# Kernel tuning notes

Hardware: AMD Instinct MI355X
Metric: run time of the kernel (lower is better)

## Reference

```python
import jax, jax.numpy as jnp
import numpy as np

T_BINS = 1000  # max_time_bins
N_HEADS = 8
BIN = 64


def _ln(x, g, b):
    m = x.mean(-1, keepdims=True)
    v = ((x - m) ** 2).mean(-1, keepdims=True)
    return (x - m) / jnp.sqrt(v + 1e-5) * g + b


def _time_attn(h, td, mask, wq, bq, wk, bk, wv, bv, wo, bo, temb):
    # h: [B,S,D], td: [B,S] float, mask: [B,S] bool
    B, S, D = h.shape
    dk = D // N_HEADS
    q = (h @ wq + bq).reshape(B, S, N_HEADS, dk)
    k = (h @ wk + bk).reshape(B, S, N_HEADS, dk)
    v = (h @ wv + bv).reshape(B, S, N_HEADS, dk)
    scores = jnp.einsum('bqhd,bkhd->bhqk', q, k) / jnp.sqrt(jnp.float32(dk))
    tb = jnp.clip(td.astype(jnp.int32), 0, T_BINS - 1)
    bias = temb[tb].transpose(0, 2, 1)[:, :, None, :]  # [B,H,1,S], key-position bias
    scores = jnp.where(mask[:, None, None, :], scores + bias, -1e9)
    attn = jax.nn.softmax(scores, axis=-1)
    ctx = jnp.einsum('bhqk,bkhd->bqhd', attn, v).reshape(B, S, D)
    return ctx @ wo + bo


def _forward(x, time_deltas,
             emb_event, emb_rel, emb_abs,
             iq_w, iq_b, ik_w, ik_b, iv_w, iv_b, io_w, io_b, i_temb, i_g, i_bt,
             eq_w, eq_b, ek_w, ek_b, ev_w, ev_b, eo_w, eo_b, e_temb, e_g, e_bt,
             w1, b1, w2, b2):
    B, S = x.shape
    NB = S // BIN  # S chosen as a multiple of bin_size -> no padding
    mask = x != 0  # padding_idx = 0
    ee = emb_event.at[0].set(0.0)  # padding_idx row is zero
    rel_bins = jnp.clip(time_deltas.astype(jnp.int32), 0, T_BINS - 1)
    abs_t = jnp.cumsum(jnp.clip(time_deltas, 0.0, None), axis=1)
    abs_bins = jnp.clip(abs_t.astype(jnp.int32), 0, T_BINS - 1)
    h = ee[x] + emb_rel[rel_bins] + emb_abs[abs_bins]  # [B,S,D]
    D = h.shape[-1]
    # intra-bin attention over [B*NB, BIN]
    hi = h.reshape(B * NB, BIN, D)
    ti = time_deltas.reshape(B * NB, BIN)
    mi = mask.reshape(B * NB, BIN)
    hi = _ln(_time_attn(hi, ti, mi, iq_w, iq_b, ik_w, ik_b, iv_w, iv_b, io_w, io_b, i_temb), i_g, i_bt)
    hi = hi.reshape(B, NB, BIN, D)
    # mean pool per bin over valid tokens
    mb = mask.reshape(B, NB, BIN)
    w = mb[..., None].astype(h.dtype)
    denom = jnp.maximum(w.sum(2), 1.0)
    bin_repr = (hi * w).sum(2) / denom  # [B,NB,D]
    bin_mask = mb.any(2)
    abs_masked = jnp.where(mb, abs_t.reshape(B, NB, BIN), 0.0)
    bin_abs = abs_masked.max(2)
    bin_rel = jnp.concatenate(
        [jnp.zeros((B, 1), h.dtype), jnp.maximum(bin_abs[:, 1:] - bin_abs[:, :-1], 0.0)], axis=1)
    h_inter = _ln(_time_attn(bin_repr, bin_rel, bin_mask,
                             eq_w, eq_b, ek_w, ek_b, ev_w, ev_b, eo_w, eo_b, e_temb), e_g, e_bt)
    last_idx = jnp.clip(bin_mask.sum(1) - 1, 0, None)
    last = h_inter[jnp.arange(B), last_idx]  # [B,D]
    return jax.nn.sigmoid(jax.nn.relu(last @ w1 + b1) @ w2 + b2)  # [B,1]


def setup_inputs() -> dict:
    key = jax.random.key(0)
    ks = jax.random.split(key, 24)
    B, S, D, V = 8, 4096, 512, 20000
    sc = 1.0 / np.sqrt(D)
    f32 = jnp.float32
    inp = {
        'x': jax.random.randint(ks[0], (B, S), 0, V),
        'time_deltas': jax.random.uniform(ks[1], (B, S), f32) * 10.0,
        'emb_event': jax.random.normal(ks[2], (V, D), f32) * 0.02,
        'emb_rel': jax.random.normal(ks[3], (T_BINS, D), f32) * 0.02,
        'emb_abs': jax.random.normal(ks[4], (T_BINS, D), f32) * 0.02,
    }
    names = ['iq', 'ik', 'iv', 'io', 'eq', 'ek', 'ev', 'eo']
    for i, n in enumerate(names):
        inp[n + '_w'] = jax.random.normal(ks[5 + i], (D, D), f32) * sc
        inp[n + '_b'] = jnp.zeros((D,), f32)
    inp['i_temb'] = jax.random.normal(ks[13], (T_BINS, N_HEADS), f32) * 0.02
    inp['e_temb'] = jax.random.normal(ks[14], (T_BINS, N_HEADS), f32) * 0.02
    inp['i_g'] = jnp.ones((D,), f32); inp['i_bt'] = jnp.zeros((D,), f32)
    inp['e_g'] = jnp.ones((D,), f32); inp['e_bt'] = jnp.zeros((D,), f32)
    inp['w1'] = jax.random.normal(ks[15], (D, D // 2), f32) * sc
    inp['b1'] = jnp.zeros((D // 2,), f32)
    inp['w2'] = jax.random.normal(ks[16], (D // 2, 1), f32) * np.sqrt(2.0 / D)
    inp['b2'] = jnp.zeros((1,), f32)
    return inp


def reference(x, time_deltas, emb_event, emb_rel, emb_abs,
              iq_w, iq_b, ik_w, ik_b, iv_w, iv_b, io_w, io_b, i_temb, i_g, i_bt,
              eq_w, eq_b, ek_w, ek_b, ev_w, ev_b, eo_w, eo_b, e_temb, e_g, e_bt,
              w1, b1, w2, b2):
    return _forward(x, time_deltas, emb_event, emb_rel, emb_abs,
                    iq_w, iq_b, ik_w, ik_b, iv_w, iv_b, io_w, io_b, i_temb, i_g, i_bt,
                    eq_w, eq_b, ek_w, ek_b, ev_w, ev_b, eo_w, eo_b, e_temb, e_g, e_bt,
                    w1, b1, w2, b2)
```

## Files before the change

### kernel.cpp

```cpp
#include <hip/hip_runtime.h>


typedef __attribute__((ext_vector_type(8))) short bf16x8;
typedef __attribute__((ext_vector_type(4))) float f32x4;
typedef __attribute__((ext_vector_type(4))) int i32x4;

#define DEVI __device__ __forceinline__

DEVI unsigned short f2bf(float f) {
  union { float f; unsigned u; } v; v.f = f;
  unsigned r = v.u + 0x7FFFu + ((v.u >> 16) & 1u);
  return (unsigned short)(r >> 16);
}
DEVI float bf2f(unsigned short u) {
  union { unsigned u; float f; } v; v.u = ((unsigned)u) << 16; return v.f;
}

#define GLOAD_LDS16(gp, lp) \
  __builtin_amdgcn_global_load_lds((const __attribute__((address_space(1))) void*)(gp), \
                                   (__attribute__((address_space(3))) void*)(lp), 16, 0, 0)

struct TPackArgs { const float* s[8]; unsigned short* d[8];
                   const float* bs[6]; float* bd[2]; };

__global__ __launch_bounds__(256) void k_tpack8(TPackArgs args) {
  __shared__ float tile[64][65];
  if (blockIdx.x == 512) {
    int t = threadIdx.x;
    for (int i = t; i < 1536; i += 256) {
      int sel = i >> 9, r = i & 511;
      args.bd[0][i] = args.bs[sel][r];
      args.bd[1][i] = args.bs[3 + sel][r];
    }
    return;
  }
  int mat = blockIdx.x >> 6;
  int tl = blockIdx.x & 63;
  const float* W = args.s[mat];
  unsigned short* Wt = args.d[mat];
  int n0 = (tl & 7) << 6, k0 = (tl >> 3) << 6;
  int t = threadIdx.x, j = t & 63, i0 = t >> 6;
#pragma unroll
  for (int rr = 0; rr < 16; ++rr) {
    int i = rr * 4 + i0;
    tile[i][j] = W[(size_t)(k0 + i) * 512 + n0 + j];
  }
  __syncthreads();
#pragma unroll
  for (int rr = 0; rr < 16; ++rr) {
    int i = rr * 4 + i0;
    Wt[(size_t)(n0 + i) * 512 + k0 + j] = f2bf(tile[j][i]);
  }
}

__global__ __launch_bounds__(64) void k_time(const float* __restrict__ td, const int* __restrict__ x,
    float* __restrict__ abs_t, float* __restrict__ bin_rel, int* __restrict__ bin_mask,
    int* __restrict__ last_idx) {
  __shared__ float tds[4096];
  __shared__ int xs[4096];
  int b = blockIdx.x, lane = threadIdx.x;
  const f32x4* tp = (const f32x4*)(td + (size_t)b * 4096);
  const i32x4* xp = (const i32x4*)(x + (size_t)b * 4096);
  for (int j = lane; j < 1024; j += 64) {
    f32x4 v = tp[j];
#pragma unroll
    for (int c = 0; c < 4; ++c) v[c] = fmaxf(v[c], 0.f);
    *(f32x4*)&tds[j * 4] = v;
    *(i32x4*)&xs[j * 4] = xp[j];
  }
  __syncthreads();
  float s = 0.f;
  for (int i = 0; i < 64; ++i) s += tds[lane * 64 + i];
  float pre = s;
#pragma unroll
  for (int off = 1; off < 64; off <<= 1) {
    float n = __shfl_up(pre, off, 64);
    if (lane >= off) pre += n;
  }
  float a = pre - s;
  float am = 0.f; int anyv = 0;
  for (int i = 0; i < 64; ++i) {
    a += tds[lane * 64 + i];
    tds[lane * 64 + i] = a;
    if (xs[lane * 64 + i] != 0) { am = fmaxf(am, a); anyv = 1; }
  }
  __syncthreads();
  float* out = abs_t + (size_t)b * 4096;
  for (int j = lane; j < 1024; j += 64)
    *(f32x4*)&out[j * 4] = *(const f32x4*)&tds[j * 4];
  float prev = __shfl_up(am, 1, 64);
  bin_rel[b * 64 + lane] = (lane == 0) ? 0.f : fmaxf(am - prev, 0.f);
  bin_mask[b * 64 + lane] = anyv;
  unsigned long long bal = __ballot(anyv != 0);
  if (lane == 0) last_idx[b] = max(__popcll(bal) - 1, 0);
}

__global__ __launch_bounds__(256) void k_embed(const int* __restrict__ x, const float* __restrict__ td,
    const float* __restrict__ abs_t, const float* __restrict__ ee, const float* __restrict__ er,
    const float* __restrict__ ea, unsigned short* __restrict__ h) {
  int t = threadIdx.x;
  int lane = t & 63;
  int c0 = lane * 8;
#pragma unroll
  for (int it = 0; it < 4; ++it) {
    int tok = blockIdx.x * 16 + it * 4 + (t >> 6);
    int xi = x[tok];
    int rb = (int)td[tok]; rb = min(max(rb, 0), 999);
    int ab = (int)abs_t[tok]; ab = min(max(ab, 0), 999);
    const f32x4* pr = (const f32x4*)(er + (size_t)rb * 512 + c0);
    const f32x4* pa = (const f32x4*)(ea + (size_t)ab * 512 + c0);
    f32x4 s0 = pr[0] + pa[0];
    f32x4 s1 = pr[1] + pa[1];
    if (xi != 0) {
      const f32x4* pe = (const f32x4*)(ee + (size_t)xi * 512 + c0);
      s0 += pe[0]; s1 += pe[1];
    }
    bf16x8 o;
#pragma unroll
    for (int i = 0; i < 4; ++i) { o[i] = (short)f2bf(s0[i]); o[4 + i] = (short)f2bf(s1[i]); }
    *(bf16x8*)(h + (size_t)tok * 512 + c0) = o;
  }
}

DEVI bf16x8 lds_frag64(const unsigned short* buf, int row, int c) {
  return *(const bf16x8*)&buf[row * 64 + ((c ^ (row & 7)) << 3)];
}

__global__ __launch_bounds__(256) void k_g128(const unsigned short* __restrict__ A,
    const unsigned short* __restrict__ Wt, const float* __restrict__ bias,
    unsigned short* __restrict__ Cout, int N, int tiles_n) {
  __shared__ unsigned short As[128 * 64];
  __shared__ unsigned short Bs[128 * 64];
  int bid = blockIdx.x;
  { int q = (int)gridDim.x >> 3; bid = (bid & 7) * q + (bid >> 3); }
  int by = bid / tiles_n, bx = bid % tiles_n;
  int m0 = by << 7, n0 = bx << 7;
  int t = threadIdx.x;
  int lane = t & 63, w = t >> 6;
  int wm = w >> 1, wn = w & 1;
  int l15 = lane & 15, l4 = lane >> 4;
  f32x4 acc[4][4] = {};
  for (int k0 = 0; k0 < 512; k0 += 64) {
    __syncthreads();
#pragma unroll
    for (int l = 0; l < 4; ++l) {
      int pos = l * 256 + t;
      int row = pos >> 3, g = (pos & 7) ^ (row & 7);
      GLOAD_LDS16(&A[(size_t)(m0 + row) * 512 + k0 + g * 8], &As[pos * 8]);
    }
#pragma unroll
    for (int l = 0; l < 4; ++l) {
      int pos = l * 256 + t;
      int row = pos >> 3, g = (pos & 7) ^ (row & 7);
      GLOAD_LDS16(&Wt[(size_t)(n0 + row) * 512 + k0 + g * 8], &Bs[pos * 8]);
    }
    __syncthreads();
#pragma unroll
    for (int ks = 0; ks < 2; ++ks) {
      bf16x8 af[4], bb[4];
#pragma unroll
      for (int i = 0; i < 4; ++i) {
        af[i] = lds_frag64(As, wm * 64 + i * 16 + l15, ks * 4 + l4);
        bb[i] = lds_frag64(Bs, wn * 64 + i * 16 + l15, ks * 4 + l4);
      }
#pragma unroll
      for (int i = 0; i < 4; ++i)
#pragma unroll
        for (int j = 0; j < 4; ++j)
          acc[i][j] = __builtin_amdgcn_mfma_f32_16x16x32_bf16(af[i], bb[j], acc[i][j], 0, 0, 0);
    }
  }
#pragma unroll
  for (int i = 0; i < 4; ++i) {
    int rowb = m0 + wm * 64 + i * 16 + ((lane >> 4) << 2);
#pragma unroll
    for (int j = 0; j < 4; ++j) {
      int col = n0 + wn * 64 + j * 16 + (lane & 15);
      float bv = bias[col];
#pragma unroll
      for (int r = 0; r < 4; ++r)
        Cout[(size_t)(rowb + r) * N + col] = f2bf(acc[i][j][r] + bv);
    }
  }
}

__global__ __launch_bounds__(512, 2) void k_oproj(const unsigned short* __restrict__ ctx,
    const unsigned short* __restrict__ WoT, const float* __restrict__ bo,
    const int* __restrict__ x, const float* __restrict__ g, const float* __restrict__ bt,
    unsigned short* __restrict__ bin_repr) {
  __shared__ unsigned short As[128 * 64];
  __shared__ unsigned short Bs[512 * 64];
  int bid = blockIdx.x;
  { int q = (int)gridDim.x >> 3; bid = (bid & 7) * q + (bid >> 3); }
  int m0 = bid << 7;
  int t = threadIdx.x;
  int lane = t & 63, w = t >> 6;
  int l15 = lane & 15, l4 = lane >> 4;

  f32x4 acc[8][4] = {};
  for (int k0 = 0; k0 < 512; k0 += 64) {
    __syncthreads();
#pragma unroll
    for (int l = 0; l < 2; ++l) {
      int pos = l * 512 + t;
      int row = pos >> 3, gg = (pos & 7) ^ (row & 7);
      GLOAD_LDS16(&ctx[(size_t)(m0 + row) * 512 + k0 + gg * 8], &As[pos * 8]);
    }
#pragma unroll
    for (int l = 0; l < 8; ++l) {
      int pos = l * 512 + t;
      int row = pos >> 3, gg = (pos & 7) ^ (row & 7);
      GLOAD_LDS16(&WoT[(size_t)row * 512 + k0 + gg * 8], &Bs[pos * 8]);
    }
    __syncthreads();
#pragma unroll
    for (int ks = 0; ks < 2; ++ks) {
      bf16x8 af[8], bb[4];
#pragma unroll
      for (int i = 0; i < 8; ++i) af[i] = lds_frag64(As, i * 16 + l15, ks * 4 + l4);
#pragma unroll
      for (int j = 0; j < 4; ++j) bb[j] = lds_frag64(Bs, w * 64 + j * 16 + l15, ks * 4 + l4);
#pragma unroll
      for (int i = 0; i < 8; ++i)
#pragma unroll
        for (int j = 0; j < 4; ++j)
          acc[i][j] = __builtin_amdgcn_mfma_f32_16x16x32_bf16(af[i], bb[j], acc[i][j], 0, 0, 0);
    }
  }

  __syncthreads();
  float* red   = (float*)&As[0];
  float* meanL = red + 128 * 9;
  float* rstdL = meanL + 128;
  int*   valL  = (int*)(rstdL + 128);
  int*   cntL  = valL + 128;

  int cols[4]; float bov[4], gv[4], bv[4];
#pragma unroll
  for (int j = 0; j < 4; ++j) {
    cols[j] = w * 64 + j * 16 + l15;
    bov[j] = bo[cols[j]]; gv[j] = g[cols[j]]; bv[j] = bt[cols[j]];
  }
  if (t < 128) {
    int v = (x[m0 + t] != 0) ? 1 : 0;
    valL[t] = v;
    unsigned long long bal = __ballot(v != 0);
    if ((t & 63) == 0) cntL[t >> 6] = __popcll(bal);
  }
#pragma unroll
  for (int i = 0; i < 8; ++i)
#pragma unroll
    for (int r = 0; r < 4; ++r) {
      float s = (acc[i][0][r] + bov[0]) + (acc[i][1][r] + bov[1]) +
                (acc[i][2][r] + bov[2]) + (acc[i][3][r] + bov[3]);
#pragma unroll
      for (int off = 1; off < 16; off <<= 1) s += __shfl_xor(s, off, 64);
      if (l15 == 0) red[(i * 16 + l4 * 4 + r) * 9 + w] = s;
    }
  __syncthreads();
  if (t < 128) {
    float m = 0.f;
#pragma unroll
    for (int ww = 0; ww < 8; ++ww) m += red[t * 9 + ww];
    meanL[t] = m * (1.f / 512.f);
  }
  __syncthreads();
#pragma unroll
  for (int i = 0; i < 8; ++i)
#pragma unroll
    for (int r = 0; r < 4; ++r) {
      float m = meanL[i * 16 + l4 * 4 + r];
      float s = 0.f;
#pragma unroll
      for (int j = 0; j < 4; ++j) { float d = acc[i][j][r] + bov[j] - m; s += d * d; }
#pragma unroll
      for (int off = 1; off < 16; off <<= 1) s += __shfl_xor(s, off, 64);
      if (l15 == 0) red[(i * 16 + l4 * 4 + r) * 9 + w] = s;
    }
  __syncthreads();
  if (t < 128) {
    float vsum = 0.f;
#pragma unroll
    for (int ww = 0; ww < 8; ++ww) vsum += red[t * 9 + ww];
    rstdL[t] = rsqrtf(vsum * (1.f / 512.f) + 1e-5f);
  }
  __syncthreads();
  float p0[4] = {0.f, 0.f, 0.f, 0.f}, p1[4] = {0.f, 0.f, 0.f, 0.f};
#pragma unroll
  for (int i = 0; i < 8; ++i)
#pragma unroll
    for (int r = 0; r < 4; ++r) {
      int row = i * 16 + l4 * 4 + r;
      if (valL[row]) {
        float m = meanL[row], rs = rstdL[row];
#pragma unroll
        for (int j = 0; j < 4; ++j) {
          float y = (acc[i][j][r] + bov[j] - m) * rs * gv[j] + bv[j];
          if (i < 4) p0[j] += y; else p1[j] += y;
        }
      }
    }
#pragma unroll
  for (int j = 0; j < 4; ++j) {
    p0[j] += __shfl_xor(p0[j], 16, 64); p0[j] += __shfl_xor(p0[j], 32, 64);
    p1[j] += __shfl_xor(p1[j], 16, 64); p1[j] += __shfl_xor(p1[j], 32, 64);
  }
  float d0 = 1.f / fmaxf((float)cntL[0], 1.f);
  float d1 = 1.f / fmaxf((float)cntL[1], 1.f);
  if (l4 == 0) {
    int binr = (m0 >> 6);
#pragma unroll
    for (int j = 0; j < 4; ++j) {
      bin_repr[(size_t)binr * 512 + cols[j]]       = f2bf(p0[j] * d0);
      bin_repr[(size_t)(binr + 1) * 512 + cols[j]] = f2bf(p1[j] * d1);
    }
  }
}

__global__ __launch_bounds__(256) void k_gemm(const unsigned short* __restrict__ A,
    const unsigned short* __restrict__ Wt, const float* __restrict__ bias,
    unsigned short* __restrict__ Cout, int N, int tiles_n) {
  __shared__ unsigned short As[128 * 72];
  __shared__ unsigned short Bs[128 * 72];
  int bx = blockIdx.x % tiles_n;
  int by = blockIdx.x / tiles_n;
  int m0 = by << 7, n0 = bx << 7;
  int t = threadIdx.x;
  int lane = t & 63, w = t >> 6;
  int wm = w >> 1, wn = w & 1;
  f32x4 acc[4][4] = {};
  for (int k0 = 0; k0 < 512; k0 += 64) {
    __syncthreads();
#pragma unroll
    for (int i = 0; i < 4; ++i) {
      int idx = t + i * 256;
      int row = idx >> 3, seg = idx & 7;
      *(bf16x8*)&As[row * 72 + seg * 8] = *(const bf16x8*)&A[(size_t)(m0 + row) * 512 + k0 + seg * 8];
      *(bf16x8*)&Bs[row * 72 + seg * 8] = *(const bf16x8*)&Wt[(size_t)(n0 + row) * 512 + k0 + seg * 8];
    }
    __syncthreads();
#pragma unroll
    for (int ks = 0; ks < 2; ++ks) {
      bf16x8 af[4], bb[4];
#pragma unroll
      for (int i = 0; i < 4; ++i) {
        af[i] = *(const bf16x8*)&As[(wm * 64 + i * 16 + (lane & 15)) * 72 + ks * 32 + (lane >> 4) * 8];
        bb[i] = *(const bf16x8*)&Bs[(wn * 64 + i * 16 + (lane & 15)) * 72 + ks * 32 + (lane >> 4) * 8];
      }
#pragma unroll
      for (int i = 0; i < 4; ++i)
#pragma unroll
        for (int j = 0; j < 4; ++j)
          acc[i][j] = __builtin_amdgcn_mfma_f32_16x16x32_bf16(af[i], bb[j], acc[i][j], 0, 0, 0);
    }
  }
#pragma unroll
  for (int i = 0; i < 4; ++i) {
    int rowb = m0 + wm * 64 + i * 16 + ((lane >> 4) << 2);
#pragma unroll
    for (int j = 0; j < 4; ++j) {
      int col = n0 + wn * 64 + j * 16 + (lane & 15);
      float bv = bias[col];
#pragma unroll
      for (int r = 0; r < 4; ++r)
        Cout[(size_t)(rowb + r) * N + col] = f2bf(acc[i][j][r] + bv);
    }
  }
}

__global__ __launch_bounds__(256) void k_attn(const unsigned short* __restrict__ qkv,
    const float* __restrict__ td, const int* __restrict__ validv,
    const float* __restrict__ temb, unsigned short* __restrict__ ctx) {
  __shared__ float bias_s[4][64];
  __shared__ int valid_s[64];
  __shared__ unsigned short P_s[4][64][72];
  __shared__ unsigned short Vt_s[4][64][72];
  int blk = blockIdx.x >> 1, hg = blockIdx.x & 1;
  int t = threadIdx.x, hl = t >> 6, lane = t & 63;
  int h = hg * 4 + hl;
  size_t base = (size_t)blk * 64;
  if (t < 64) {
    valid_s[t] = (validv[base + t] != 0) ? 1 : 0;
    int tb = (int)td[base + t];
    tb = min(max(tb, 0), 999);
#pragma unroll
    for (int hh = 0; hh < 4; ++hh) bias_s[hh][t] = temb[tb * 8 + hg * 4 + hh];
  }
  {
    const unsigned short* vp = qkv + (base + lane) * 1536 + 1024 + h * 64;
#pragma unroll
    for (int f8 = 0; f8 < 8; ++f8) {
      bf16x8 v8 = *(const bf16x8*)(vp + f8 * 8);
#pragma unroll
      for (int j = 0; j < 8; ++j) Vt_s[hl][f8 * 8 + j][lane] = (unsigned short)v8[j];
    }
  }
  __syncthreads();
  bf16x8 qa[2][4], kb[2][4];
#pragma unroll
  for (int ks = 0; ks < 2; ++ks)
#pragma unroll
    for (int i = 0; i < 4; ++i) {
      int row = i * 16 + (lane & 15);
      int kk = ks * 32 + (lane >> 4) * 8;
      qa[ks][i] = *(const bf16x8*)&qkv[(base + row) * 1536 + h * 64 + kk];
      kb[ks][i] = *(const bf16x8*)&qkv[(base + row) * 1536 + 512 + h * 64 + kk];
    }
  f32x4 acc[4][4] = {};
#pragma unroll
  for (int ks = 0; ks < 2; ++ks)
#pragma unroll
    for (int i = 0; i < 4; ++i)
#pragma unroll
      for (int j = 0; j < 4; ++j)
        acc[i][j] = __builtin_amdgcn_mfma_f32_16x16x32_bf16(qa[ks][i], kb[ks][j], acc[i][j], 0, 0, 0);
  float invs[4][4];
#pragma unroll
  for (int i = 0; i < 4; ++i) {
#pragma unroll
    for (int r = 0; r < 4; ++r) {
      float sv[4];
#pragma unroll
      for (int j = 0; j < 4; ++j) {
        int key = j * 16 + (lane & 15);
        float s = acc[i][j][r] * 0.125f;
        sv[j] = valid_s[key] ? (s + bias_s[hl][key]) : -1e9f;
      }
      float m = fmaxf(fmaxf(sv[0], sv[1]), fmaxf(sv[2], sv[3]));
#pragma unroll
      for (int off = 1; off < 16; off <<= 1) m = fmaxf(m, __shfl_xor(m, off, 64));
      float p[4], sum = 0.f;
#pragma unroll
      for (int j = 0; j < 4; ++j) { p[j] = __expf(sv[j] - m); sum += p[j]; }
#pragma unroll
      for (int off = 1; off < 16; off <<= 1) sum += __shfl_xor(sum, off, 64);
      invs[i][r] = 1.f / sum;
      int row = i * 16 + ((lane >> 4) << 2) + r;
#pragma unroll
      for (int j = 0; j < 4; ++j) P_s[hl][row][j * 16 + (lane & 15)] = f2bf(p[j]);
    }
  }
  __syncthreads();
  f32x4 acc2[4][4] = {};
#pragma unroll
  for (int ks = 0; ks < 2; ++ks) {
    bf16x8 pa[4], vb[4];
    int kk = ks * 32 + (lane >> 4) * 8;
#pragma unroll
    for (int i = 0; i < 4; ++i) {
      pa[i] = *(const bf16x8*)&P_s[hl][i * 16 + (lane & 15)][kk];
      vb[i] = *(const bf16x8*)&Vt_s[hl][i * 16 + (lane & 15)][kk];
    }
#pragma unroll
    for (int i = 0; i < 4; ++i)
#pragma unroll
      for (int j = 0; j < 4; ++j)
        acc2[i][j] = __builtin_amdgcn_mfma_f32_16x16x32_bf16(pa[i], vb[j], acc2[i][j], 0, 0, 0);
  }
#pragma unroll
  for (int i = 0; i < 4; ++i) {
    int rowb = i * 16 + ((lane >> 4) << 2);
#pragma unroll
    for (int j = 0; j < 4; ++j) {
      int col = h * 64 + j * 16 + (lane & 15);
#pragma unroll
      for (int r = 0; r < 4; ++r)
        ctx[(base + rowb + r) * 512 + col] = f2bf(acc2[i][j][r] * invs[i][r]);
    }
  }
}

__global__ __launch_bounds__(256) void k_final(const unsigned short* __restrict__ proj2,
    const int* __restrict__ last_idx, const float* __restrict__ g, const float* __restrict__ bt,
    const float* __restrict__ w1, const float* __restrict__ b1,
    const float* __restrict__ w2, const float* __restrict__ b2, float* __restrict__ outp) {
  __shared__ float row_s[512];
  __shared__ float red_s[4];
  __shared__ float red2_s[4];
  int b = blockIdx.x, t = threadIdx.x;
  const unsigned short* rp = proj2 + (size_t)(b * 64 + last_idx[b]) * 512;
  float v0 = bf2f(rp[t]), v1 = bf2f(rp[t + 256]);
  float s = v0 + v1;
#pragma unroll
  for (int off = 1; off < 64; off <<= 1) s += __shfl_xor(s, off, 64);
  if ((t & 63) == 0) red_s[t >> 6] = s;
  __syncthreads();
  float mean = (red_s[0] + red_s[1] + red_s[2] + red_s[3]) * (1.f / 512.f);
  float d0 = v0 - mean, d1 = v1 - mean;
  float vs = d0 * d0 + d1 * d1;
#pragma unroll
  for (int off = 1; off < 64; off <<= 1) vs += __shfl_xor(vs, off, 64);
  if ((t & 63) == 0) red2_s[t >> 6] = vs;
  __syncthreads();
  float rstd = rsqrtf((red2_s[0] + red2_s[1] + red2_s[2] + red2_s[3]) * (1.f / 512.f) + 1e-5f);
  row_s[t]       = d0 * rstd * g[t]       + bt[t];
  row_s[t + 256] = d1 * rstd * g[t + 256] + bt[t + 256];
  __syncthreads();
  float acc = b1[t];
  for (int k = 0; k < 512; ++k) acc += row_s[k] * w1[(size_t)k * 256 + t];
  float hv = fmaxf(acc, 0.f) * w2[t];
#pragma unroll
  for (int off = 1; off < 64; off <<= 1) hv += __shfl_xor(hv, off, 64);
  if ((t & 63) == 0) red_s[t >> 6] = hv;
  __syncthreads();
  if (t == 0) {
    float o = red_s[0] + red_s[1] + red_s[2] + red_s[3] + b2[0];
    outp[b] = 1.f / (1.f + __expf(-o));
  }
}

extern "C" void kernel_launch(void* const* d_in, const int* in_sizes, int n_in,
                              void* d_out, int out_size, void* d_ws, size_t ws_size,
                              hipStream_t stream) {
  const int*   x    = (const int*)d_in[0];
  const float* td   = (const float*)d_in[1];
  const float* ee   = (const float*)d_in[2];
  const float* er   = (const float*)d_in[3];
  const float* ea   = (const float*)d_in[4];
  const float* iq_w = (const float*)d_in[5];  const float* iq_b = (const float*)d_in[6];
  const float* ik_w = (const float*)d_in[7];  const float* ik_b = (const float*)d_in[8];
  const float* iv_w = (const float*)d_in[9];  const float* iv_b = (const float*)d_in[10];
  const float* io_w = (const float*)d_in[11]; const float* io_b = (const float*)d_in[12];
  const float* eq_w = (const float*)d_in[13]; const float* eq_b = (const float*)d_in[14];
  const float* ek_w = (const float*)d_in[15]; const float* ek_b = (const float*)d_in[16];
  const float* ev_w = (const float*)d_in[17]; const float* ev_b = (const float*)d_in[18];
  const float* eo_w = (const float*)d_in[19]; const float* eo_b = (const float*)d_in[20];
  const float* i_temb = (const float*)d_in[21];
  const float* e_temb = (const float*)d_in[22];
  const float* i_g  = (const float*)d_in[23]; const float* i_bt = (const float*)d_in[24];
  const float* e_g  = (const float*)d_in[25]; const float* e_bt = (const float*)d_in[26];
  const float* w1   = (const float*)d_in[27]; const float* b1   = (const float*)d_in[28];
  const float* w2   = (const float*)d_in[29]; const float* b2   = (const float*)d_in[30];

  char* ws = (char*)d_ws;
  size_t off = 0;
  auto alloc = [&](size_t nb) { size_t r = off; off += (nb + 255) & ~(size_t)255; return r; };
  float* abs_t    = (float*)(ws + alloc((size_t)32768 * 4));
  float* bin_rel  = (float*)(ws + alloc(512 * 4));
  int*   bin_mask = (int*)(ws + alloc(512 * 4));
  int*   last_idx = (int*)(ws + alloc(64));
  unsigned short* wqkv_i = (unsigned short*)(ws + alloc((size_t)1536 * 512 * 2));
  unsigned short* wo_i   = (unsigned short*)(ws + alloc((size_t)512 * 512 * 2));
  unsigned short* wqkv_e = (unsigned short*)(ws + alloc((size_t)1536 * 512 * 2));
  unsigned short* wo_e   = (unsigned short*)(ws + alloc((size_t)512 * 512 * 2));
  float* bqkv_i = (float*)(ws + alloc(1536 * 4));
  float* bqkv_e = (float*)(ws + alloc(1536 * 4));
  unsigned short* hbuf = (unsigned short*)(ws + alloc((size_t)32768 * 512 * 2));
  unsigned short* qkvbuf = (unsigned short*)(ws + alloc((size_t)32768 * 1536 * 2));
  unsigned short* bin_repr = (unsigned short*)(ws + alloc((size_t)512 * 512 * 2));
  char* small = ws + alloc((size_t)512 * 1536 * 2);
  unsigned short* qkv2 = (unsigned short*)small;
  unsigned short* proj2 = (unsigned short*)small;
  unsigned short* ctx2 = (unsigned short*)(ws + alloc((size_t)512 * 512 * 2));

  TPackArgs tp;
  tp.s[0] = iq_w; tp.d[0] = wqkv_i;
  tp.s[1] = ik_w; tp.d[1] = wqkv_i + (size_t)512 * 512;
  tp.s[2] = iv_w; tp.d[2] = wqkv_i + (size_t)1024 * 512;
  tp.s[3] = io_w; tp.d[3] = wo_i;
  tp.s[4] = eq_w; tp.d[4] = wqkv_e;
  tp.s[5] = ek_w; tp.d[5] = wqkv_e + (size_t)512 * 512;
  tp.s[6] = ev_w; tp.d[6] = wqkv_e + (size_t)1024 * 512;
  tp.s[7] = eo_w; tp.d[7] = wo_e;
  tp.bs[0] = iq_b; tp.bs[1] = ik_b; tp.bs[2] = iv_b;
  tp.bs[3] = eq_b; tp.bs[4] = ek_b; tp.bs[5] = ev_b;
  tp.bd[0] = bqkv_i; tp.bd[1] = bqkv_e;
  k_tpack8<<<513, 256, 0, stream>>>(tp);

  k_time<<<8, 64, 0, stream>>>(td, x, abs_t, bin_rel, bin_mask, last_idx);

  k_embed<<<2048, 256, 0, stream>>>(x, td, abs_t, ee, er, ea, hbuf);

  k_g128<<<256 * 12, 256, 0, stream>>>(hbuf, wqkv_i, bqkv_i, qkvbuf, 1536, 12);
  k_attn<<<1024, 256, 0, stream>>>(qkvbuf, td, x, i_temb, hbuf);
  k_oproj<<<256, 512, 0, stream>>>(hbuf, wo_i, io_b, x, i_g, i_bt, bin_repr);

  k_gemm<<<4 * 12, 256, 0, stream>>>(bin_repr, wqkv_e, bqkv_e, qkv2, 1536, 12);
  k_attn<<<16, 256, 0, stream>>>(qkv2, bin_rel, bin_mask, e_temb, ctx2);
  k_gemm<<<4 * 4, 256, 0, stream>>>(ctx2, wo_e, eo_b, proj2, 512, 4);

  k_final<<<8, 256, 0, stream>>>(proj2, last_idx, e_g, e_bt, w1, b1, w2, b2, (float*)d_out);
}
```

Measured before the change: 238.5 us.

## Replace QKV GEMM with 256x256 multi-stage pipelined kernel and coalesced epilogues

```diff
diff --git a/kernel.cpp b/kernel.cpp
--- a/kernel.cpp
+++ b/kernel.cpp
@@ -122,64 +122,118 @@
   }
 }
 
+DEVI bf16x8 lds_frag32(const unsigned short* buf, int r, int g) {
+  int sr = r >> 1;
+  int slot = (((r & 1) << 2) | g) ^ (sr & 7);
+  return *(const bf16x8*)&buf[sr * 64 + slot * 8];
+}
 DEVI bf16x8 lds_frag64(const unsigned short* buf, int row, int c) {
   return *(const bf16x8*)&buf[row * 64 + ((c ^ (row & 7)) << 3)];
 }
 
-__global__ __launch_bounds__(256) void k_g128(const unsigned short* __restrict__ A,
+__global__ __launch_bounds__(512, 2) void k_gemm256(const unsigned short* __restrict__ A,
     const unsigned short* __restrict__ Wt, const float* __restrict__ bias,
     unsigned short* __restrict__ Cout, int N, int tiles_n) {
-  __shared__ unsigned short As[128 * 64];
-  __shared__ unsigned short Bs[128 * 64];
+  __shared__ unsigned short lds[4][2][256 * 32];
   int bid = blockIdx.x;
   { int q = (int)gridDim.x >> 3; bid = (bid & 7) * q + (bid >> 3); }
   int by = bid / tiles_n, bx = bid % tiles_n;
-  int m0 = by << 7, n0 = bx << 7;
+  int m0 = by << 8, n0 = bx << 8;
   int t = threadIdx.x;
   int lane = t & 63, w = t >> 6;
-  int wm = w >> 1, wn = w & 1;
+  int wm = w >> 2, wn = w & 3;
   int l15 = lane & 15, l4 = lane >> 4;
-  f32x4 acc[4][4] = {};
-  for (int k0 = 0; k0 < 512; k0 += 64) {
-    __syncthreads();
-#pragma unroll
-    for (int l = 0; l < 4; ++l) {
-      int pos = l * 256 + t;
-      int row = pos >> 3, g = (pos & 7) ^ (row & 7);
-      GLOAD_LDS16(&A[(size_t)(m0 + row) * 512 + k0 + g * 8], &As[pos * 8]);
-    }
-#pragma unroll
-    for (int l = 0; l < 4; ++l) {
-      int pos = l * 256 + t;
-      int row = pos >> 3, g = (pos & 7) ^ (row & 7);
-      GLOAD_LDS16(&Wt[(size_t)(n0 + row) * 512 + k0 + g * 8], &Bs[pos * 8]);
-    }
-    __syncthreads();
-#pragma unroll
-    for (int ks = 0; ks < 2; ++ks) {
-      bf16x8 af[4], bb[4];
-#pragma unroll
-      for (int i = 0; i < 4; ++i) {
-        af[i] = lds_frag64(As, wm * 64 + i * 16 + l15, ks * 4 + l4);
-        bb[i] = lds_frag64(Bs, wn * 64 + i * 16 + l15, ks * 4 + l4);
-      }
-#pragma unroll
-      for (int i = 0; i < 4; ++i)
-#pragma unroll
-        for (int j = 0; j < 4; ++j)
-          acc[i][j] = __builtin_amdgcn_mfma_f32_16x16x32_bf16(af[i], bb[j], acc[i][j], 0, 0, 0);
-    }
-  }
-#pragma unroll
-  for (int i = 0; i < 4; ++i) {
-    int rowb = m0 + wm * 64 + i * 16 + ((lane >> 4) << 2);
-#pragma unroll
-    for (int j = 0; j < 4; ++j) {
-      int col = n0 + wn * 64 + j * 16 + (lane & 15);
-      float bv = bias[col];
-#pragma unroll
-      for (int r = 0; r < 4; ++r)
-        Cout[(size_t)(rowb + r) * N + col] = f2bf(acc[i][j][r] + bv);
+
+  auto stageA = [&](int kt) {
+    int k0 = kt << 5;
+    unsigned short* dst = &lds[kt & 3][0][0];
+#pragma unroll
+    for (int l = 0; l < 2; ++l) {
+      int pos = l * 512 + t;
+      int sr = pos >> 3, slot = pos & 7;
+      int gp = slot ^ (sr & 7);
+      int row = sr * 2 + (gp >> 2);
+      GLOAD_LDS16(&A[(size_t)(m0 + row) * 512 + k0 + (gp & 3) * 8], dst + pos * 8);
+    }
+  };
+  auto stageB = [&](int kt) {
+    int k0 = kt << 5;
+    unsigned short* dst = &lds[kt & 3][1][0];
+#pragma unroll
+    for (int l = 0; l < 2; ++l) {
+      int pos = l * 512 + t;
+      int sr = pos >> 3, slot = pos & 7;
+      int gp = slot ^ (sr & 7);
+      int row = sr * 2 + (gp >> 2);
+      GLOAD_LDS16(&Wt[(size_t)(n0 + row) * 512 + k0 + (gp & 3) * 8], dst + pos * 8);
+    }
+  };
+
+  f32x4 acc[8][4] = {};
+  stageA(0); stageB(0);
+  stageA(1); stageB(1);
+  stageA(2); stageB(2);
+
+  for (int kt = 0; kt < 16; ++kt) {
+    if (kt < 14)       asm volatile("s_waitcnt vmcnt(8)" ::: "memory");
+    else if (kt == 14) asm volatile("s_waitcnt vmcnt(4)" ::: "memory");
+    else               asm volatile("s_waitcnt vmcnt(0)" ::: "memory");
+    __builtin_amdgcn_s_barrier();
+    const unsigned short* As = &lds[kt & 3][0][0];
+    const unsigned short* Bs = &lds[kt & 3][1][0];
+
+    bf16x8 af[4], bb[4];
+#pragma unroll
+    for (int i = 0; i < 4; ++i) af[i] = lds_frag32(As, wm * 128 + i * 16 + l15, l4);
+#pragma unroll
+    for (int j = 0; j < 4; ++j) bb[j] = lds_frag32(Bs, wn * 64 + j * 16 + l15, l4);
+    if (kt < 13) stageA(kt + 3);
+    __builtin_amdgcn_s_barrier();
+    asm volatile("s_waitcnt lgkmcnt(0)" ::: "memory");
+    __builtin_amdgcn_sched_barrier(0);
+    __builtin_amdgcn_s_setprio(1);
+#pragma unroll
+    for (int i = 0; i < 4; ++i)
+#pragma unroll
+      for (int j = 0; j < 4; ++j)
+        acc[i][j] = __builtin_amdgcn_mfma_f32_16x16x32_bf16(af[i], bb[j], acc[i][j], 0, 0, 0);
+    __builtin_amdgcn_s_setprio(0);
+
+    bf16x8 ah[4];
+#pragma unroll
+    for (int i = 0; i < 4; ++i) ah[i] = lds_frag32(As, wm * 128 + 64 + i * 16 + l15, l4);
+    if (kt < 13) stageB(kt + 3);
+    __builtin_amdgcn_s_barrier();
+    asm volatile("s_waitcnt lgkmcnt(0)" ::: "memory");
+    __builtin_amdgcn_sched_barrier(0);
+    __builtin_amdgcn_s_setprio(1);
+#pragma unroll
+    for (int i = 0; i < 4; ++i)
+#pragma unroll
+      for (int j = 0; j < 4; ++j)
+        acc[4 + i][j] = __builtin_amdgcn_mfma_f32_16x16x32_bf16(ah[i], bb[j], acc[4 + i][j], 0, 0, 0);
+    __builtin_amdgcn_s_setprio(0);
+  }
+
+  __syncthreads();
+  unsigned short* scr = ((unsigned short*)lds) + (size_t)w * 4352;
+  float bov[4];
+#pragma unroll
+  for (int j = 0; j < 4; ++j) bov[j] = bias[n0 + wn * 64 + j * 16 + l15];
+#pragma unroll
+  for (int c = 0; c < 2; ++c) {
+#pragma unroll
+    for (int i = 0; i < 4; ++i)
+#pragma unroll
+      for (int j = 0; j < 4; ++j)
+#pragma unroll
+        for (int r = 0; r < 4; ++r)
+          scr[(i * 16 + l4 * 4 + r) * 68 + j * 16 + l15] = f2bf(acc[c * 4 + i][j][r] + bov[j]);
+#pragma unroll
+    for (int p = 0; p < 8; ++p) {
+      int rl = p * 8 + (lane >> 3);
+      bf16x8 vv = *(const bf16x8*)&scr[rl * 68 + (lane & 7) * 8];
+      *(bf16x8*)&Cout[(size_t)(m0 + wm * 128 + c * 64 + rl) * N + n0 + wn * 64 + (lane & 7) * 8] = vv;
     }
   }
 }
@@ -457,16 +511,20 @@
       for (int j = 0; j < 4; ++j)
         acc2[i][j] = __builtin_amdgcn_mfma_f32_16x16x32_bf16(pa[i], vb[j], acc2[i][j], 0, 0, 0);
   }
-#pragma unroll
-  for (int i = 0; i < 4; ++i) {
-    int rowb = i * 16 + ((lane >> 4) << 2);
-#pragma unroll
-    for (int j = 0; j < 4; ++j) {
-      int col = h * 64 + j * 16 + (lane & 15);
+  unsigned short* scr = &Vt_s[hl][0][0];
+#pragma unroll
+  for (int i = 0; i < 4; ++i)
+#pragma unroll
+    for (int j = 0; j < 4; ++j)
 #pragma unroll
       for (int r = 0; r < 4; ++r)
-        ctx[(base + rowb + r) * 512 + col] = f2bf(acc2[i][j][r] * invs[i][r]);
-    }
+        scr[(i * 16 + ((lane >> 4) << 2) + r) * 72 + j * 16 + (lane & 15)] =
+            f2bf(acc2[i][j][r] * invs[i][r]);
+#pragma unroll
+  for (int p = 0; p < 8; ++p) {
+    int rl = p * 8 + (lane >> 3);
+    bf16x8 vv = *(const bf16x8*)&scr[rl * 72 + (lane & 7) * 8];
+    *(bf16x8*)&ctx[(base + rl) * 512 + h * 64 + (lane & 7) * 8] = vv;
   }
 }
 
@@ -571,7 +629,7 @@
 
   k_embed<<<2048, 256, 0, stream>>>(x, td, abs_t, ee, er, ea, hbuf);
 
-  k_g128<<<256 * 12, 256, 0, stream>>>(hbuf, wqkv_i, bqkv_i, qkvbuf, 1536, 12);
+  k_gemm256<<<128 * 6, 512, 0, stream>>>(hbuf, wqkv_i, bqkv_i, qkvbuf, 1536, 6);
   k_attn<<<1024, 256, 0, stream>>>(qkvbuf, td, x, i_temb, hbuf);
   k_oproj<<<256, 512, 0, stream>>>(hbuf, wo_i, io_b, x, i_g, i_bt, bin_repr);
 
```

After: 237.7 us. About the same (-0.4%).
